# Kernel tuning notes

Hardware: AMD Instinct MI355X
Metric: run time of the kernel (lower is better)

Reference implementation:

```python
import jax, jax.numpy as jnp
import numpy as np

N = 10000
E = 320000
IN_DIM = 128
HID = 64


def setup_inputs() -> dict:
    key = jax.random.key(0)
    k1, k2, k3, k4 = jax.random.split(key, 4)
    x = jax.random.normal(k1, (N, IN_DIM), dtype=jnp.float32)
    edge_index = jax.random.randint(k2, (2, E), 0, N, dtype=jnp.int64)
    # Glorot-style init for GCN linear weights
    W1 = jax.random.normal(k3, (IN_DIM, HID), dtype=jnp.float32) * (1.0 / np.sqrt(IN_DIM))
    b1 = jnp.zeros((HID,), dtype=jnp.float32)
    W2 = jax.random.normal(k4, (HID, HID), dtype=jnp.float32) * (1.0 / np.sqrt(HID))
    b2 = jnp.zeros((HID,), dtype=jnp.float32)
    return {"x": x, "edge_index": edge_index, "W1": W1, "b1": b1, "W2": W2, "b2": b2}


def gcn_conv(x, src, dst, W, b, n_nodes):
    # PyG GCNConv: add self-loops, symmetric normalization D^-1/2 (A+I) D^-1/2, XW + b
    xw = x @ W                                           # [N, H]
    deg = jax.ops.segment_sum(jnp.ones_like(dst, dtype=x.dtype), dst,
                              num_segments=n_nodes)      # [N]
    deg_inv_sqrt = jnp.where(deg > 0, jax.lax.rsqrt(deg), 0.0)
    norm = deg_inv_sqrt[src] * deg_inv_sqrt[dst]         # [E+N]
    msg = xw[src] * norm[:, None]                        # gather + scale
    out = jax.ops.segment_sum(msg, dst, num_segments=n_nodes)  # scatter-add
    return out + b


def reference(x, edge_index, W1, b1, W2, b2):
    n_nodes = x.shape[0]
    loops = jnp.arange(n_nodes, dtype=edge_index.dtype)
    src = jnp.concatenate([edge_index[0], loops])
    dst = jnp.concatenate([edge_index[1], loops])
    h = jax.nn.relu(gcn_conv(x, src, dst, W1, b1, n_nodes))
    h = gcn_conv(h, src, dst, W2, b2, n_nodes)
    prob_adj = jax.nn.sigmoid(h @ h.T)                   # [N, N] dense
    return prob_adj
```

## Files before the change

### kernel.cpp

```cpp
#include <hip/hip_runtime.h>
#include <hip/hip_bf16.h>

#define NN 10000
#define INDIM 128
#define HID 64
#define CAP 96
#define CB 1250
#define GB 2500

typedef __attribute__((ext_vector_type(8))) short bf16x8;
typedef __attribute__((ext_vector_type(4))) float f32x4;

__global__ __launch_bounds__(256) void k_build_gemm1(
    const int* __restrict__ dst, int E, int* __restrict__ cnt,
    int* __restrict__ bucket, const int* __restrict__ src,
    const float* __restrict__ x, const float* __restrict__ W1,
    float* __restrict__ xw) {
  __shared__ float w[INDIM * HID];
  int b = blockIdx.x, t = threadIdx.x;
  if (b < CB) {
    int e = b * 256 + t;
    if (e < E) {
      int d = dst[e];
      int p = atomicAdd(&cnt[d], 1);
      if (p < CAP) bucket[d * CAP + p] = src[e];
    }
  } else {
    for (int i = t; i < INDIM * HID; i += 256) w[i] = W1[i];
    __syncthreads();
    int r = (b - CB) * 4 + (t >> 6);
    int j = t & 63;
    float2 xv = ((const float2*)(x + (size_t)r * INDIM))[j & (INDIM / 2 - 1)];
    float acc = 0.f;
    #pragma unroll
    for (int k = 0; k < INDIM; k++) {
      float xk = __shfl((k & 1) ? xv.y : xv.x, k >> 1, 64);
      acc = fmaf(xk, w[k * HID + j], acc);
    }
    xw[(size_t)r * HID + j] = acc;
  }
}

__global__ __launch_bounds__(256) void k_agg1_gemm2(
    const float* __restrict__ xw, const int* __restrict__ cnt,
    const int* __restrict__ bucket, const float* __restrict__ b1,
    const float* __restrict__ W2, float* __restrict__ hB) {
  __shared__ float w[HID * HID];
  int t = threadIdx.x;
  for (int i = t; i < HID * HID; i += 256) w[i] = W2[i];
  __syncthreads();
  int wid = t >> 6, lane = t & 63;
  int d = blockIdx.x * 4 + wid;
  int c = cnt[d];
  float dis_d = rsqrtf((float)(c + 1));
  int deg = c < CAP ? c : CAP;
  const int* bk = bucket + (size_t)d * CAP;
  float acc = xw[(size_t)d * HID + lane] * dis_d;
  int k = 0;
  for (; k + 8 <= deg; k += 8) {
    int i0 = bk[k],     i1 = bk[k + 1], i2 = bk[k + 2], i3 = bk[k + 3];
    int i4 = bk[k + 4], i5 = bk[k + 5], i6 = bk[k + 6], i7 = bk[k + 7];
    float s0 = rsqrtf((float)(cnt[i0] + 1)), s1 = rsqrtf((float)(cnt[i1] + 1));
    float s2 = rsqrtf((float)(cnt[i2] + 1)), s3 = rsqrtf((float)(cnt[i3] + 1));
    float s4 = rsqrtf((float)(cnt[i4] + 1)), s5 = rsqrtf((float)(cnt[i5] + 1));
    float s6 = rsqrtf((float)(cnt[i6] + 1)), s7 = rsqrtf((float)(cnt[i7] + 1));
    float v0 = xw[(size_t)i0 * HID + lane], v1 = xw[(size_t)i1 * HID + lane];
    float v2 = xw[(size_t)i2 * HID + lane], v3 = xw[(size_t)i3 * HID + lane];
    float v4 = xw[(size_t)i4 * HID + lane], v5 = xw[(size_t)i5 * HID + lane];
    float v6 = xw[(size_t)i6 * HID + lane], v7 = xw[(size_t)i7 * HID + lane];
    acc += v0 * s0 + v1 * s1 + v2 * s2 + v3 * s3
         + v4 * s4 + v5 * s5 + v6 * s6 + v7 * s7;
  }
  for (; k < deg; k++) {
    int s = bk[k];
    acc = fmaf(xw[(size_t)s * HID + lane], rsqrtf((float)(cnt[s] + 1)), acc);
  }
  float h = fmaxf(acc * dis_d + b1[lane], 0.f);
  float acc2 = 0.f;
  #pragma unroll
  for (int kk = 0; kk < HID; kk++)
    acc2 = fmaf(__shfl(h, kk, 64), w[kk * HID + lane], acc2);
  hB[(size_t)d * HID + lane] = acc2 * dis_d;
}

__global__ __launch_bounds__(256) void k_agg2(
    const float* __restrict__ hB, const int* __restrict__ cnt,
    const int* __restrict__ bucket, const float* __restrict__ b2,
    __hip_bfloat16* __restrict__ h2b) {
  int t = threadIdx.x, wid = t >> 6, lane = t & 63;
  int d = blockIdx.x * 4 + wid;
  int c = cnt[d];
  float dis_d = rsqrtf((float)(c + 1));
  int deg = c < CAP ? c : CAP;
  const int* bk = bucket + (size_t)d * CAP;
  float acc = hB[(size_t)d * HID + lane];
  int k = 0;
  for (; k + 8 <= deg; k += 8) {
    int i0 = bk[k],     i1 = bk[k + 1], i2 = bk[k + 2], i3 = bk[k + 3];
    int i4 = bk[k + 4], i5 = bk[k + 5], i6 = bk[k + 6], i7 = bk[k + 7];
    float v0 = hB[(size_t)i0 * HID + lane], v1 = hB[(size_t)i1 * HID + lane];
    float v2 = hB[(size_t)i2 * HID + lane], v3 = hB[(size_t)i3 * HID + lane];
    float v4 = hB[(size_t)i4 * HID + lane], v5 = hB[(size_t)i5 * HID + lane];
    float v6 = hB[(size_t)i6 * HID + lane], v7 = hB[(size_t)i7 * HID + lane];
    acc += ((v0 + v1) + (v2 + v3)) + ((v4 + v5) + (v6 + v7));
  }
  for (; k < deg; k++) acc += hB[(size_t)bk[k] * HID + lane];
  float v = acc * dis_d + b2[lane];
  h2b[(size_t)d * HID + lane] = __float2bfloat16(v);
}

__global__ __launch_bounds__(256) void k_final(const short* __restrict__ hb,
                                               float* __restrict__ out) {
  const int T = (NN + 63) / 64;
  int wid = threadIdx.x >> 6, lane = threadIdx.x & 63;
  int tx = blockIdx.x * 2 + (wid & 1);
  int ty = blockIdx.y * 2 + (wid >> 1);
  if (tx >= T || ty >= T) return;
  int rowbase = tx * 64, colbase = ty * 64;
  int m = lane & 15, q = lane >> 4;

  bf16x8 a0[4], a1[4], b0[4], b1[4];
  #pragma unroll
  for (int rt = 0; rt < 4; rt++) {
    int r = rowbase + rt * 16 + m; r = r < NN ? r : NN - 1;
    const bf16x8* p = reinterpret_cast<const bf16x8*>(hb + (size_t)r * HID + q * 8);
    a0[rt] = p[0]; a1[rt] = p[4];
  }
  #pragma unroll
  for (int ct = 0; ct < 4; ct++) {
    int r = colbase + ct * 16 + m; r = r < NN ? r : NN - 1;
    const bf16x8* p = reinterpret_cast<const bf16x8*>(hb + (size_t)r * HID + q * 8);
    b0[ct] = p[0]; b1[ct] = p[4];
  }

  f32x4 acc[4][4];
  #pragma unroll
  for (int rt = 0; rt < 4; rt++)
    #pragma unroll
    for (int ct = 0; ct < 4; ct++) {
      f32x4 z = {0.f, 0.f, 0.f, 0.f};
      z = __builtin_amdgcn_mfma_f32_16x16x32_bf16(a0[rt], b0[ct], z, 0, 0, 0);
      z = __builtin_amdgcn_mfma_f32_16x16x32_bf16(a1[rt], b1[ct], z, 0, 0, 0);
      acc[rt][ct] = z;
    }

  #pragma unroll
  for (int ct = 0; ct < 4; ct++)
    #pragma unroll
    for (int rt = 0; rt < 4; rt++) {
      if (rowbase + rt * 16 < NN && colbase + ct * 16 < NN) {
        f32x4 z = acc[rt][ct], o;
        #pragma unroll
        for (int j = 0; j < 4; j++)
          o[j] = __builtin_amdgcn_rcpf(1.0f + __expf(-z[j]));
        size_t orow = (size_t)(colbase + ct * 16 + m);
        size_t ocol = (size_t)(rowbase + rt * 16 + q * 4);
        *reinterpret_cast<f32x4*>(out + orow * NN + ocol) = o;
      }
    }
}

extern "C" void kernel_launch(void* const* d_in, const int* in_sizes, int n_in,
                              void* d_out, int out_size, void* d_ws, size_t ws_size,
                              hipStream_t stream) {
  const float* x  = (const float*)d_in[0];
  const int*   ei = (const int*)d_in[1];
  const float* W1 = (const float*)d_in[2];
  const float* b1 = (const float*)d_in[3];
  const float* W2 = (const float*)d_in[4];
  const float* b2 = (const float*)d_in[5];
  int E = in_sizes[1] / 2;
  const int* src = ei;
  const int* dst = ei + E;

  char* base = (char*)d_out;
  float* xw     = (float*)(base);
  float* hB     = (float*)(base + 2560000);
  int*   bucket = (int*)(base + 5120000);
  int*   cnt    = (int*)(base + 5120000 + (size_t)NN * CAP * 4);
  __hip_bfloat16* h2b = (__hip_bfloat16*)d_ws;

  hipMemsetAsync(cnt, 0, NN * sizeof(int), stream);
  k_build_gemm1<<<CB + GB, 256, 0, stream>>>(dst, E, cnt, bucket, src,
                                             x, W1, xw);
  k_agg1_gemm2<<<NN / 4, 256, 0, stream>>>(xw, cnt, bucket, b1, W2, hB);
  k_agg2<<<NN / 4, 256, 0, stream>>>(hB, cnt, bucket, b2, h2b);

  const int T = (NN + 63) / 64;
  dim3 gf((T + 1) / 2, (T + 1) / 2);
  k_final<<<gf, 256, 0, stream>>>((const short*)h2b, (float*)d_out);
}
```

Before: 167.5 us.

## Restructure final outer-product kernel into row bands with looped column tiles

```diff
diff --git a/kernel.cpp b/kernel.cpp
--- a/kernel.cpp
+++ b/kernel.cpp
@@ -111,53 +111,29 @@
 
 __global__ __launch_bounds__(256) void k_final(const short* __restrict__ hb,
                                                float* __restrict__ out) {
-  const int T = (NN + 63) / 64;
-  int wid = threadIdx.x >> 6, lane = threadIdx.x & 63;
-  int tx = blockIdx.x * 2 + (wid & 1);
-  int ty = blockIdx.y * 2 + (wid >> 1);
-  if (tx >= T || ty >= T) return;
-  int rowbase = tx * 64, colbase = ty * 64;
+  int t = threadIdx.x, wid = t >> 6, lane = t & 63;
   int m = lane & 15, q = lane >> 4;
+  int ro = blockIdx.y * 16;
+  int start = blockIdx.x * 157;
+  int end = start + 157; if (end > 625) end = 625;
 
-  bf16x8 a0[4], a1[4], b0[4], b1[4];
-  #pragma unroll
-  for (int rt = 0; rt < 4; rt++) {
-    int r = rowbase + rt * 16 + m; r = r < NN ? r : NN - 1;
-    const bf16x8* p = reinterpret_cast<const bf16x8*>(hb + (size_t)r * HID + q * 8);
-    a0[rt] = p[0]; a1[rt] = p[4];
+  const bf16x8* pb = reinterpret_cast<const bf16x8*>(hb + (size_t)(ro + m) * HID + q * 8);
+  bf16x8 b0 = pb[0], b1 = pb[4];
+
+  #pragma unroll 2
+  for (int ct = start + wid; ct < end; ct += 4) {
+    int ci = ct * 16;
+    const bf16x8* pa = reinterpret_cast<const bf16x8*>(hb + (size_t)(ci + m) * HID + q * 8);
+    bf16x8 a0 = pa[0], a1 = pa[4];
+    f32x4 z = {0.f, 0.f, 0.f, 0.f};
+    z = __builtin_amdgcn_mfma_f32_16x16x32_bf16(a0, b0, z, 0, 0, 0);
+    z = __builtin_amdgcn_mfma_f32_16x16x32_bf16(a1, b1, z, 0, 0, 0);
+    f32x4 o;
+    #pragma unroll
+    for (int j = 0; j < 4; j++)
+      o[j] = __builtin_amdgcn_rcpf(1.0f + __expf(-z[j]));
+    *reinterpret_cast<f32x4*>(out + (size_t)(ro + m) * NN + ci + q * 4) = o;
   }
-  #pragma unroll
-  for (int ct = 0; ct < 4; ct++) {
-    int r = colbase + ct * 16 + m; r = r < NN ? r : NN - 1;
-    const bf16x8* p = reinterpret_cast<const bf16x8*>(hb + (size_t)r * HID + q * 8);
-    b0[ct] = p[0]; b1[ct] = p[4];
-  }
-
-  f32x4 acc[4][4];
-  #pragma unroll
-  for (int rt = 0; rt < 4; rt++)
-    #pragma unroll
-    for (int ct = 0; ct < 4; ct++) {
-      f32x4 z = {0.f, 0.f, 0.f, 0.f};
-      z = __builtin_amdgcn_mfma_f32_16x16x32_bf16(a0[rt], b0[ct], z, 0, 0, 0);
-      z = __builtin_amdgcn_mfma_f32_16x16x32_bf16(a1[rt], b1[ct], z, 0, 0, 0);
-      acc[rt][ct] = z;
-    }
-
-  #pragma unroll
-  for (int ct = 0; ct < 4; ct++)
-    #pragma unroll
-    for (int rt = 0; rt < 4; rt++) {
-      if (rowbase + rt * 16 < NN && colbase + ct * 16 < NN) {
-        f32x4 z = acc[rt][ct], o;
-        #pragma unroll
-        for (int j = 0; j < 4; j++)
-          o[j] = __builtin_amdgcn_rcpf(1.0f + __expf(-z[j]));
-        size_t orow = (size_t)(colbase + ct * 16 + m);
-        size_t ocol = (size_t)(rowbase + rt * 16 + q * 4);
-        *reinterpret_cast<f32x4*>(out + orow * NN + ocol) = o;
-      }
-    }
 }
 
 extern "C" void kernel_launch(void* const* d_in, const int* in_sizes, int n_in,
@@ -186,7 +162,6 @@
   k_agg1_gemm2<<<NN / 4, 256, 0, stream>>>(xw, cnt, bucket, b1, W2, hB);
   k_agg2<<<NN / 4, 256, 0, stream>>>(hB, cnt, bucket, b2, h2b);
 
-  const int T = (NN + 63) / 64;
-  dim3 gf((T + 1) / 2, (T + 1) / 2);
+  dim3 gf(4, NN / 16);
   k_final<<<gf, 256, 0, stream>>>((const short*)h2b, (float*)d_out);
 }
```

After: 201.0 us. 20.0% more time.
